# Performance work log

Hardware: AMD Instinct MI355X
Metric: run time of the kernel (lower is better)

Reference implementation:

```python
import jax, jax.numpy as jnp
import numpy as np
import math

H = 16          # attn_heads
DK = 64         # features_dec // attn_heads
NEG = -1e9      # additive causal mask value
EPS = 1e-6      # LayerNorm eps (annotated transformer)


def get_slopes(n):
    def p2(m):
        start = 2.0 ** (-(2.0 ** (-(math.log2(m) - 3))))
        return [start * start ** i for i in range(m)]
    if math.log2(n).is_integer():
        return p2(n)
    cp = 2 ** math.floor(math.log2(n))
    return p2(cp) + get_slopes(2 * cp)[0::2][: n - cp]


def setup_inputs() -> dict:
    key = jax.random.key(0)
    ks = jax.random.split(key, 12)
    B, S, FT, FDZ, FDEC, FD = 8, 1024, 16, 768, 1024, 16

    def lin(k, out_d, in_d):
        return jax.random.normal(k, (out_d, in_d), jnp.float32) / np.float32(np.sqrt(in_d))

    return {
        "z_sample": jax.random.normal(ks[0], (B, FDZ), jnp.float32),
        "r_traj": jax.random.normal(ks[1], (B, S, FT), jnp.float32),
        "dense_w": lin(ks[2], FDEC, FDZ + FT), "dense_b": jnp.zeros((FDEC,), jnp.float32),
        "ln_g": jnp.ones((FDEC,), jnp.float32), "ln_b": jnp.zeros((FDEC,), jnp.float32),
        "wq": lin(ks[3], FDEC, FDEC), "bq": jnp.zeros((FDEC,), jnp.float32),
        "wk": lin(ks[4], FDEC, FDEC), "bk": jnp.zeros((FDEC,), jnp.float32),
        "wv": lin(ks[5], FDEC, FDEC), "bv": jnp.zeros((FDEC,), jnp.float32),
        "wo": lin(ks[6], FDEC, FDEC), "bo": jnp.zeros((FDEC,), jnp.float32),
        "dec_w": lin(ks[7], FD, FDEC), "dec_b": jnp.zeros((FD,), jnp.float32),
    }


def reference(z_sample, r_traj, dense_w, dense_b, ln_g, ln_b,
              wq, bq, wk, bk, wv, bv, wo, bo, dec_w, dec_b):
    B, S, _ = r_traj.shape
    # concat trajectory features with broadcast latent sample -> [B,S,in_size]
    x = jnp.concatenate(
        [r_traj, jnp.broadcast_to(z_sample[:, None, :], (B, S, z_sample.shape[-1]))], axis=-1)
    x = x @ dense_w.T + dense_b  # [B,S,FDEC]

    # causal additive mask + ALiBi bias: bias[h,i,j] = causal(i,j) + slope_h * j
    slopes = jnp.asarray(get_slopes(H), jnp.float32)
    causal = jnp.triu(jnp.full((S, S), NEG, jnp.float32), k=1)
    bias = causal[None, :, :] + slopes[:, None, None] * jnp.arange(S, dtype=jnp.float32)[None, None, :]  # [H,S,S]

    # pre-norm sublayer: x + attn(LN(x))  (dropout=0 / eval)
    mu = x.mean(-1, keepdims=True)
    var = x.var(-1, keepdims=True)
    xn = ln_g * (x - mu) / jnp.sqrt(var + EPS) + ln_b

    def heads(w, b):
        return (xn @ w.T + b).reshape(B, S, H, DK).transpose(0, 2, 1, 3)  # [B,H,S,DK]

    q, k, v = heads(wq, bq), heads(wk, bk), heads(wv, bv)
    scores = jnp.einsum('bhid,bhjd->bhij', q, k) / np.float32(np.sqrt(DK)) + bias[None]
    attn = jax.nn.softmax(scores, axis=-1)
    o = jnp.einsum('bhij,bhjd->bhid', attn, v).transpose(0, 2, 1, 3).reshape(B, S, H * DK)
    x = x + o @ wo.T + bo

    # decode_state then transpose(-2,-1) -> [B, features_d, S]
    return (x @ dec_w.T + dec_b).transpose(0, 2, 1)
```

## Files before the change

### kernel.cpp

```cpp
#include <hip/hip_runtime.h>

static constexpr int Bn   = 8;
static constexpr int S    = 1024;
static constexpr int FT   = 16;
static constexpr int FDZ  = 768;
static constexpr int INK  = 784;
static constexpr int FDEC = 1024;
static constexpr int M    = Bn * S;
static constexpr int H    = 16;
static constexpr int FD   = 16;

typedef __bf16 bf16x8 __attribute__((ext_vector_type(8)));
typedef float  f32x4  __attribute__((ext_vector_type(4)));

__device__ __forceinline__ unsigned short f2b(float f) {
  return __builtin_bit_cast(unsigned short, static_cast<__bf16>(f));
}
__device__ __forceinline__ float b2f(unsigned short u) {
  return (float)__builtin_bit_cast(__bf16, u);
}

__device__ __forceinline__ void gload16(const void* g, void* l) {
  __builtin_amdgcn_global_load_lds(
      (const __attribute__((address_space(1))) unsigned int*)g,
      (__attribute__((address_space(3))) unsigned int*)l, 16, 0, 0);
}

__global__ __launch_bounds__(256) void k_pre(const float* __restrict__ dnw,
                                             const float* __restrict__ wq,
                                             const float* __restrict__ wk,
                                             const float* __restrict__ wv,
                                             const float* __restrict__ wo,
                                             const float* __restrict__ dcw,
                                             const float* __restrict__ bq,
                                             const float* __restrict__ bk,
                                             const float* __restrict__ bv,
                                             const float* __restrict__ bo,
                                             const float* __restrict__ dcb,
                                             const float* __restrict__ z,
                                             unsigned short* __restrict__ w3,
                                             unsigned short* __restrict__ dwb,
                                             float* __restrict__ b3,
                                             unsigned short* __restrict__ wt16,
                                             float* __restrict__ part,
                                             float* __restrict__ bias2,
                                             float* __restrict__ za) {
  const int bid = blockIdx.x, tid = threadIdx.x;
  const int c = tid * 4;
  if (bid < 3072) {
    const int r = bid;
    const float* src = (r < 1024) ? wq : (r < 2048 ? wk : wv);
    const int rr = r & 1023;
    float4 v = *reinterpret_cast<const float4*>(&src[(size_t)rr * 1024 + c]);
    unsigned short o4[4] = {f2b(v.x), f2b(v.y), f2b(v.z), f2b(v.w)};
    *reinterpret_cast<uint2*>(&w3[(size_t)r * 1024 + c]) = *reinterpret_cast<uint2*>(o4);
  } else if (bid < 3088) {
    const int r = bid - 3072;
    float4 v = *reinterpret_cast<const float4*>(&dcw[(size_t)r * 1024 + c]);
    unsigned short o4[4] = {f2b(v.x), f2b(v.y), f2b(v.z), f2b(v.w)};
    *reinterpret_cast<uint2*>(&dwb[(size_t)r * 1024 + c]) = *reinterpret_cast<uint2*>(o4);
  } else if (bid < 3091) {
    const int r = bid - 3088;
    const float* s = (r == 0) ? bq : (r == 1 ? bk : bv);
    *reinterpret_cast<float4*>(&b3[r * 1024 + c]) =
        *reinterpret_cast<const float4*>(&s[c]);
  } else if (bid < 3155) {
    const int idx = (bid - 3091) * 256 + tid;
    const int k = idx >> 10, cc = idx & 1023;
    wt16[k * 1024 + cc] = f2b(dnw[(size_t)cc * INK + k]);
  } else if (bid < 3219) {
    const int kb = bid - 3155;
    const int k0 = kb * 16;
    float4 wv4[16];
#pragma unroll
    for (int k = 0; k < 16; k++)
      wv4[k] = *reinterpret_cast<const float4*>(&wo[(size_t)(k0 + k) * 1024 + c]);
#pragma unroll
    for (int i = 0; i < 16; i++) {
      float4 a = make_float4(0.f, 0.f, 0.f, 0.f);
#pragma unroll
      for (int k = 0; k < 16; k++) {
        float d = dcw[i * 1024 + k0 + k];
        a.x += d * wv4[k].x; a.y += d * wv4[k].y;
        a.z += d * wv4[k].z; a.w += d * wv4[k].w;
      }
      *reinterpret_cast<float4*>(&part[((size_t)kb * 16 + i) * 1024 + c]) = a;
    }
  } else if (bid < 3220) {
    const int lane = tid & 63, w = tid >> 6;
    for (int q = 0; q < 4; q++) {
      int f = w * 4 + q;
      const float* dp = &dcw[(size_t)f * 1024];
      float s = 0.f;
#pragma unroll
      for (int t = 0; t < 16; t++) {
        int k = lane + t * 64;
        s += dp[k] * bo[k];
      }
      for (int off = 32; off; off >>= 1) s += __shfl_down(s, off);
      if (lane == 0) bias2[f] = s + dcb[f];
    }
  } else {
    const int lane = tid & 63, w = tid >> 6;
    const int idx = (bid - 3220) * 4 + w;
    const int col = idx >> 3, b = idx & 7;
    const float* wp = &dnw[(size_t)col * INK + FT];
    const float* zp = &z[b * FDZ];
    float s = 0.f;
#pragma unroll
    for (int i = 0; i < 12; i++) {
      int k = lane + i * 64;
      s += wp[k] * zp[k];
    }
    for (int off = 32; off; off >>= 1) s += __shfl_down(s, off);
    if (lane == 0) za[b * 1024 + col] = s;
  }
}

__global__ __launch_bounds__(256) void k_dln(const float* __restrict__ rt,
                                             const float* __restrict__ za,
                                             const float* __restrict__ dnb,
                                             const float* __restrict__ lng,
                                             const float* __restrict__ lnb,
                                             const unsigned short* __restrict__ wt16g,
                                             const float* __restrict__ part,
                                             unsigned short* __restrict__ xres,
                                             unsigned short* __restrict__ xn,
                                             unsigned short* __restrict__ wcombb) {
  const int tid = threadIdx.x;
  if (blockIdx.x >= 2048) {
    const int idx = (blockIdx.x - 2048) * 256 + tid;
    float s = 0.f;
#pragma unroll 8
    for (int kb = 0; kb < 64; kb++) s += part[(size_t)kb * 16384 + idx];
    wcombb[idx] = f2b(s);
    return;
  }
  __shared__ unsigned short wt[16 * 1024];
  __shared__ float ss[4], qq[4];
  const int lane = tid & 63, wv = tid >> 6;
  const int c0 = tid * 4;
#pragma unroll
  for (int i = 0; i < 8; i++)
    reinterpret_cast<uint4*>(wt)[tid + 256 * i] =
        reinterpret_cast<const uint4*>(wt16g)[tid + 256 * i];
  const float4 bv  = *reinterpret_cast<const float4*>(&dnb[c0]);
  const float4 gv  = *reinterpret_cast<const float4*>(&lng[c0]);
  const float4 bev = *reinterpret_cast<const float4*>(&lnb[c0]);
  __syncthreads();

  for (int r = 0; r < 4; ++r) {
    const int m = blockIdx.x * 4 + r;
    const int b = m >> 10;
    float rtv[16];
    {
      float4 t0 = *reinterpret_cast<const float4*>(&rt[m * 16 + 0]);
      float4 t1 = *reinterpret_cast<const float4*>(&rt[m * 16 + 4]);
      float4 t2 = *reinterpret_cast<const float4*>(&rt[m * 16 + 8]);
      float4 t3 = *reinterpret_cast<const float4*>(&rt[m * 16 + 12]);
      rtv[0]=t0.x; rtv[1]=t0.y; rtv[2]=t0.z; rtv[3]=t0.w;
      rtv[4]=t1.x; rtv[5]=t1.y; rtv[6]=t1.z; rtv[7]=t1.w;
      rtv[8]=t2.x; rtv[9]=t2.y; rtv[10]=t2.z; rtv[11]=t2.w;
      rtv[12]=t3.x; rtv[13]=t3.y; rtv[14]=t3.z; rtv[15]=t3.w;
    }
    float4 zav = *reinterpret_cast<const float4*>(&za[b * 1024 + c0]);
    float acc[4] = {zav.x + bv.x, zav.y + bv.y, zav.z + bv.z, zav.w + bv.w};
#pragma unroll
    for (int k = 0; k < 16; ++k) {
      uint2 wraw = *reinterpret_cast<const uint2*>(&wt[k * 1024 + c0]);
      const unsigned short* wp = reinterpret_cast<const unsigned short*>(&wraw);
      float rk = rtv[k];
      acc[0] += rk * b2f(wp[0]);
      acc[1] += rk * b2f(wp[1]);
      acc[2] += rk * b2f(wp[2]);
      acc[3] += rk * b2f(wp[3]);
    }
    float s = acc[0] + acc[1] + acc[2] + acc[3];
    float q = acc[0]*acc[0] + acc[1]*acc[1] + acc[2]*acc[2] + acc[3]*acc[3];
    for (int off = 32; off; off >>= 1) { s += __shfl_down(s, off); q += __shfl_down(q, off); }
    if (lane == 0) { ss[wv] = s; qq[wv] = q; }
    __syncthreads();
    float St = ss[0] + ss[1] + ss[2] + ss[3];
    float Qt = qq[0] + qq[1] + qq[2] + qq[3];
    float mu  = St * (1.f / 1024.f);
    float var = Qt * (1.f / 1024.f) - mu * mu;
    float rstd = rsqrtf(var + 1e-6f);
    unsigned short xo[4], no[4];
    xo[0] = f2b(acc[0]); no[0] = f2b(gv.x * (acc[0] - mu) * rstd + bev.x);
    xo[1] = f2b(acc[1]); no[1] = f2b(gv.y * (acc[1] - mu) * rstd + bev.y);
    xo[2] = f2b(acc[2]); no[2] = f2b(gv.z * (acc[2] - mu) * rstd + bev.z);
    xo[3] = f2b(acc[3]); no[3] = f2b(gv.w * (acc[3] - mu) * rstd + bev.w);
    *reinterpret_cast<uint2*>(&xres[(size_t)m * 1024 + c0]) = *reinterpret_cast<uint2*>(xo);
    *reinterpret_cast<uint2*>(&xn[(size_t)m * 1024 + c0])   = *reinterpret_cast<uint2*>(no);
    __syncthreads();
  }
}

template<int EPI>
__global__ __launch_bounds__(256, 3) void k_gemm1(const unsigned short* __restrict__ A, int lda,
                                                  const unsigned short* __restrict__ Bw, int ldb,
                                                  int K, int N,
                                                  const float* __restrict__ bias,
                                                  unsigned short* __restrict__ Cb) {
  __shared__ __align__(16) unsigned short As[3 * 128 * 32];
  __shared__ __align__(16) unsigned short Bs[3 * 128 * 32];
  const int tid = threadIdx.x, lane = tid & 63, w = tid >> 6;
  const int wr = w >> 1, wc = w & 1;
  const int lr = lane & 15, lg = lane >> 4;

  const int xcd = blockIdx.x & 7;
  const int j   = blockIdx.x >> 3;
  const int m0  = (xcd * 8 + (j & 7)) * 128;
  const int n0  = (j >> 3) * 128;

  const int nt = K >> 5;

  const int g0 = tid;
  const int r0g = g0 >> 2, c0g = (g0 & 3) ^ ((r0g >> 1) & 3);
  const int g1 = tid + 256;
  const int r1g = g1 >> 2, c1g = (g1 & 3) ^ ((r1g >> 1) & 3);
  const unsigned short* srcA0 = A + (size_t)(m0 + r0g) * lda + c0g * 8;
  const unsigned short* srcA1 = A + (size_t)(m0 + r1g) * lda + c1g * 8;
  const unsigned short* srcB0 = Bw + (size_t)(n0 + r0g) * ldb + c0g * 8;
  const unsigned short* srcB1 = Bw + (size_t)(n0 + r1g) * ldb + c1g * 8;
  const int d0 = (w * 64) * 8;
  const int d1 = (256 + w * 64) * 8;

  int offA[4], offB[4];
#pragma unroll
  for (int mi = 0; mi < 4; mi++) {
    int r = wr * 64 + mi * 16 + lr;
    offA[mi] = r * 32 + (lg ^ ((r >> 1) & 3)) * 8;
  }
#pragma unroll
  for (int ni = 0; ni < 4; ni++) {
    int r = wc * 64 + ni * 16 + lr;
    offB[ni] = r * 32 + (lg ^ ((r >> 1) & 3)) * 8;
  }

  f32x4 acc[4][4];
#pragma unroll
  for (int i = 0; i < 4; i++)
#pragma unroll
    for (int j2 = 0; j2 < 4; j2++)
#pragma unroll
      for (int e = 0; e < 4; e++) acc[i][j2][e] = 0.f;

  auto stage = [&](int tt) {
    const int sl = tt % 3;
    const size_t ko = (size_t)tt * 32;
    gload16(srcA0 + ko, &As[sl * 4096 + d0]);
    gload16(srcA1 + ko, &As[sl * 4096 + d1]);
    gload16(srcB0 + ko, &Bs[sl * 4096 + d0]);
    gload16(srcB1 + ko, &Bs[sl * 4096 + d1]);
  };
  auto compute = [&](int tt) {
    const int sl = (tt % 3) * 4096;
    bf16x8 af[4], bfr[4];
#pragma unroll
    for (int mi = 0; mi < 4; mi++)
      af[mi] = *reinterpret_cast<const bf16x8*>(&As[sl + offA[mi]]);
#pragma unroll
    for (int ni = 0; ni < 4; ni++)
      bfr[ni] = *reinterpret_cast<const bf16x8*>(&Bs[sl + offB[ni]]);
    __builtin_amdgcn_s_setprio(1);
#pragma unroll
    for (int mi = 0; mi < 4; mi++)
#pragma unroll
      for (int ni = 0; ni < 4; ni++)
        acc[mi][ni] = __builtin_amdgcn_mfma_f32_16x16x32_bf16(af[mi], bfr[ni], acc[mi][ni], 0, 0, 0);
    __builtin_amdgcn_s_setprio(0);
  };

  stage(0); stage(1);

  int t = 0;
  for (; t < nt - 2; ++t) {
    asm volatile("s_waitcnt vmcnt(4)" ::: "memory");
    __builtin_amdgcn_s_barrier();
    stage(t + 2);
    compute(t);
  }
  asm volatile("s_waitcnt vmcnt(4)" ::: "memory");
  __builtin_amdgcn_s_barrier();
  compute(t); ++t;
  asm volatile("s_waitcnt vmcnt(0)" ::: "memory");
  __builtin_amdgcn_s_barrier();
  compute(t);

#pragma unroll
  for (int mi = 0; mi < 4; mi++)
#pragma unroll
    for (int ni = 0; ni < 4; ni++) {
      int col = n0 + wc * 64 + ni * 16 + lr;
      float bv = bias ? bias[col] : 0.f;
#pragma unroll
      for (int jj = 0; jj < 4; jj++) {
        int row = m0 + wr * 64 + mi * 16 + lg * 4 + jj;
        float v = acc[mi][ni][jj] + bv;
        Cb[(size_t)row * N + col] = f2b(v);
      }
    }
}

__global__ __launch_bounds__(512, 4) void k_attn(const unsigned short* __restrict__ qkv,
                                                 unsigned short* __restrict__ o) {
  __shared__ unsigned short Ks[2][64][72];
  __shared__ unsigned short Vt[2][64][72];
  __shared__ unsigned short Pl[8][16][72];
  const int tid = threadIdx.x, lane = tid & 63, w = tid >> 6;
  const int bh = blockIdx.x, b = bh >> 4, h = bh & 15;
  const int lr = lane & 15, lg = lane >> 4, lg4 = lg * 4;
  const int krow = tid >> 3, c8 = (tid & 7) << 3;
  const int kb8 = krow >> 3, kl = krow & 7, vq = tid & 7;
  const float slope2 = exp2f(-0.5f * (float)(h + 1)) * 1.44269504f;
  const float sc2 = 0.125f * 1.44269504f;

  const int y = blockIdx.y;
  const int qloA = y * 128 + w * 16;
  const int qloB = (7 - y) * 128 + w * 16;
  const int qaA = qloA + lr, qaB = qloB + lr;

  bf16x8 qfA0, qfA1, qfB0, qfB1;
  {
    const unsigned short* qp = &qkv[(size_t)(b * 1024 + qloA + lr) * 3072 + h * 64];
    qfA0 = *reinterpret_cast<const bf16x8*>(qp + lg * 8);
    qfA1 = *reinterpret_cast<const bf16x8*>(qp + 32 + lg * 8);
    const unsigned short* qp2 = &qkv[(size_t)(b * 1024 + qloB + lr) * 3072 + h * 64];
    qfB0 = *reinterpret_cast<const bf16x8*>(qp2 + lg * 8);
    qfB1 = *reinterpret_cast<const bf16x8*>(qp2 + 32 + lg * 8);
  }
  float mrunA = -3.0e38f, lrunA = 0.f, mrunB = -3.0e38f, lrunB = 0.f;
  f32x4 accOA[4], accOB[4];
  for (int dn = 0; dn < 4; dn++)
    for (int e = 0; e < 4; e++) { accOA[dn][e] = 0.f; accOB[dn][e] = 0.f; }

  const int nt = 16 - 2 * y;

  auto proc = [&](int kb, int cb, int qlo, int qa, float& mrun, float& lrun,
                  f32x4 (&accO)[4], bf16x8 qf0, bf16x8 qf1) {
    f32x4 sf[4];
    for (int kn = 0; kn < 4; kn++) {
      f32x4 zz;
      for (int e = 0; e < 4; e++) zz[e] = 0.f;
      bf16x8 kf0 = *reinterpret_cast<const bf16x8*>(&Ks[cb][kn * 16 + lr][lg * 8]);
      bf16x8 kf1 = *reinterpret_cast<const bf16x8*>(&Ks[cb][kn * 16 + lr][32 + lg * 8]);
      zz = __builtin_amdgcn_mfma_f32_16x16x32_bf16(kf0, qf0, zz, 0, 0, 0);
      zz = __builtin_amdgcn_mfma_f32_16x16x32_bf16(kf1, qf1, zz, 0, 0, 0);
      sf[kn] = zz;
    }
    const bool needmask = (kb + 63 > qlo);
    float sc[4][4];
    float ml = -3.0e38f;
    for (int kn = 0; kn < 4; kn++) {
      float alib = slope2 * (float)(kb + kn * 16 + lg4);
      for (int jj = 0; jj < 4; jj++) {
        float v = fmaf(sf[kn][jj], sc2, alib + slope2 * (float)jj);
        if (needmask && (kb + kn * 16 + lg4 + jj > qa)) v = -3.0e38f;
        sc[kn][jj] = v;
        ml = fmaxf(ml, v);
      }
    }
    ml = fmaxf(ml, __shfl_xor(ml, 16));
    ml = fmaxf(ml, __shfl_xor(ml, 32));
    float mnew = fmaxf(mrun, ml);
    float f = exp2f(mrun - mnew);
    float rs = 0.f;
    for (int kn = 0; kn < 4; kn++) {
      __bf16 pb[4];
      for (int jj = 0; jj < 4; jj++) {
        float pv = exp2f(sc[kn][jj] - mnew);
        rs += pv;
        pb[jj] = (__bf16)pv;
      }
      *reinterpret_cast<uint2*>(&Pl[w][lr][kn * 16 + lg4]) =
          *reinterpret_cast<uint2*>(pb);
    }
    rs += __shfl_xor(rs, 16);
    rs += __shfl_xor(rs, 32);
    lrun = lrun * f + rs;
    mrun = mnew;
    float fj[4];
    for (int jj = 0; jj < 4; jj++) fj[jj] = __shfl(f, (lane & 48) | (lg4 + jj));
    for (int dn = 0; dn < 4; dn++)
      for (int jj = 0; jj < 4; jj++) accO[dn][jj] *= fj[jj];
    asm volatile("s_waitcnt lgkmcnt(0)" ::: "memory");
    for (int ks = 0; ks < 2; ks++) {
      bf16x8 pa = *reinterpret_cast<const bf16x8*>(&Pl[w][lr][ks * 32 + lg * 8]);
      for (int dn = 0; dn < 4; dn++) {
        int d = dn * 16 + lr;
        bf16x8 vb = *reinterpret_cast<const bf16x8*>(
            &Vt[cb][d][(((ks * 4 + lg) ^ (d >> 3)) << 3)]);
        accO[dn] = __builtin_amdgcn_mfma_f32_16x16x32_bf16(pa, vb, accO[dn], 0, 0, 0);
      }
    }
  };

  uint4 kr, vr;
  {
    const size_t base = (size_t)(b * 1024 + krow) * 3072 + h * 64;
    kr = *reinterpret_cast<const uint4*>(&qkv[base + 1024 + c8]);
    vr = *reinterpret_cast<const uint4*>(&qkv[base + 2048 + c8]);
  }
  *reinterpret_cast<uint4*>(&Ks[0][krow][c8]) = kr;
  {
    const unsigned short* vs = reinterpret_cast<const unsigned short*>(&vr);
    for (int jj = 0; jj < 8; jj++)
      Vt[0][c8 + jj][((kb8 ^ vq) << 3) | kl] = vs[jj];
  }
  __syncthreads();

  for (int kt = 0; kt < nt; ++kt) {
    const int kb = kt << 6;
    const int cb = kt & 1, nb = cb ^ 1;
    const bool hn = (kt + 1 < nt);
    if (hn) {
      const size_t base = (size_t)(b * 1024 + kb + 64 + krow) * 3072 + h * 64;
      kr = *reinterpret_cast<const uint4*>(&qkv[base + 1024 + c8]);
      vr = *reinterpret_cast<const uint4*>(&qkv[base + 2048 + c8]);
    }
    if (kb <= qloA + 15)
      proc(kb, cb, qloA, qaA, mrunA, lrunA, accOA, qfA0, qfA1);
    if (hn) {
      *reinterpret_cast<uint4*>(&Ks[nb][krow][c8]) = kr;
      const unsigned short* vs = reinterpret_cast<const unsigned short*>(&vr);
      for (int jj = 0; jj < 8; jj++)
        Vt[nb][c8 + jj][((kb8 ^ vq) << 3) | kl] = vs[jj];
    }
    if (kb <= qloB + 15)
      proc(kb, cb, qloB, qaB, mrunB, lrunB, accOB, qfB0, qfB1);
    __syncthreads();
  }

  float linvA[4], linvB[4];
  for (int jj = 0; jj < 4; jj++) {
    linvA[jj] = 1.f / __shfl(lrunA, (lane & 48) | (lg4 + jj));
    linvB[jj] = 1.f / __shfl(lrunB, (lane & 48) | (lg4 + jj));
  }
  for (int dn = 0; dn < 4; dn++)
    for (int jj = 0; jj < 4; jj++) {
      int d = dn * 16 + lr;
      int rowA = qloA + lg4 + jj;
      o[(size_t)(b * 1024 + rowA) * 1024 + h * 64 + d] = f2b(accOA[dn][jj] * linvA[jj]);
      int rowB = qloB + lg4 + jj;
      o[(size_t)(b * 1024 + rowB) * 1024 + h * 64 + d] = f2b(accOB[dn][jj] * linvB[jj]);
    }
}

__global__ __launch_bounds__(256) void k_dec2(const unsigned short* __restrict__ xres,
                                              const unsigned short* __restrict__ ob,
                                              const unsigned short* __restrict__ dwb,
                                              const unsigned short* __restrict__ wcombb,
                                              const float* __restrict__ bias2,
                                              float* __restrict__ out) {
  const int tid = threadIdx.x, lane = tid & 63, w = tid >> 6;
  const int lr = lane & 15, lg = lane >> 4;
  const int sb = blockIdx.x * 4 + w;
  const int r0 = sb * 16;
  f32x4 acc;
  for (int e = 0; e < 4; e++) acc[e] = 0.f;
  const unsigned short* arow1 = &xres[(size_t)(r0 + lr) * 1024];
  const unsigned short* arow2 = &ob[(size_t)(r0 + lr) * 1024];
  const unsigned short* brow1 = &dwb[(size_t)lr * 1024];
  const unsigned short* brow2 = &wcombb[(size_t)lr * 1024];
  for (int k0 = 0; k0 < 1024; k0 += 32) {
    bf16x8 a1 = *reinterpret_cast<const bf16x8*>(arow1 + k0 + lg * 8);
    bf16x8 b1 = *reinterpret_cast<const bf16x8*>(brow1 + k0 + lg * 8);
    acc = __builtin_amdgcn_mfma_f32_16x16x32_bf16(a1, b1, acc, 0, 0, 0);
    bf16x8 a2 = *reinterpret_cast<const bf16x8*>(arow2 + k0 + lg * 8);
    bf16x8 b2 = *reinterpret_cast<const bf16x8*>(brow2 + k0 + lg * 8);
    acc = __builtin_amdgcn_mfma_f32_16x16x32_bf16(a2, b2, acc, 0, 0, 0);
  }
  const int b = r0 >> 10;
  const int sl = (r0 & 1023) + lg * 4;
  float bias = bias2[lr];
  float4 res;
  res.x = acc[0] + bias; res.y = acc[1] + bias; res.z = acc[2] + bias; res.w = acc[3] + bias;
  *reinterpret_cast<float4*>(&out[(size_t)(b * 16 + lr) * 1024 + sl]) = res;
}

extern "C" void kernel_launch(void* const* d_in, const int* in_sizes, int n_in,
                              void* d_out, int out_size, void* d_ws, size_t ws_size,
                              hipStream_t stream) {
  (void)in_sizes; (void)n_in; (void)out_size;
  const float* z   = (const float*)d_in[0];
  const float* rt  = (const float*)d_in[1];
  const float* dnw = (const float*)d_in[2];
  const float* dnb = (const float*)d_in[3];
  const float* lng = (const float*)d_in[4];
  const float* lnb = (const float*)d_in[5];
  const float* wq  = (const float*)d_in[6];
  const float* bq  = (const float*)d_in[7];
  const float* wk  = (const float*)d_in[8];
  const float* bk  = (const float*)d_in[9];
  const float* wv  = (const float*)d_in[10];
  const float* bv  = (const float*)d_in[11];
  const float* wo  = (const float*)d_in[12];
  const float* bo  = (const float*)d_in[13];
  const float* dcw = (const float*)d_in[14];
  const float* dcb = (const float*)d_in[15];
  float* out = (float*)d_out;

  char* p = (char*)d_ws;
  unsigned short* xres  = (unsigned short*)p; p += (size_t)M * FDEC * 2;
  unsigned short* xn    = (unsigned short*)p; p += (size_t)M * FDEC * 2;
  unsigned short* w3    = (unsigned short*)p; p += (size_t)3 * FDEC * FDEC * 2;
  float* b3             = (float*)p;          p += (size_t)3 * FDEC * 4;
  unsigned short* qkv   = (unsigned short*)p; p += (size_t)M * 3 * FDEC * 2;
  unsigned short* ob    = (unsigned short*)p; p += (size_t)M * FDEC * 2;
  unsigned short* dwb   = (unsigned short*)p; p += (size_t)FD * FDEC * 2;
  unsigned short* wcombb= (unsigned short*)p; p += (size_t)FD * FDEC * 2;
  float* bias2          = (float*)p;          p += (size_t)FD * 4;
  float* za             = (float*)p;          p += (size_t)8 * 1024 * 4;
  unsigned short* wt16  = (unsigned short*)p; p += (size_t)16 * 1024 * 2;
  float* part           = (float*)p;          p += (size_t)64 * FD * FDEC * 4;
  if ((size_t)(p - (char*)d_ws) > ws_size) return;

  k_pre<<<5268, 256, 0, stream>>>(dnw, wq, wk, wv, wo, dcw, bq, bk, bv, bo, dcb, z,
                                  w3, dwb, b3, wt16, part, bias2, za);
  k_dln<<<2112, 256, 0, stream>>>(rt, za, dnb, lng, lnb, wt16, part, xres, xn, wcombb);
  k_gemm1<1><<<(M / 128) * (3 * FDEC / 128), 256, 0, stream>>>(xn, FDEC, w3, FDEC, FDEC, 3 * FDEC, b3, qkv);
  k_attn<<<dim3(Bn * H, 4), 512, 0, stream>>>(qkv, ob);
  k_dec2<<<M / 64, 256, 0, stream>>>(xres, ob, dwb, wcombb, bias2, out);
}
```

Before: 159.9 us.

## Fuse folded output projection into attention epilogue with atomic accumulation

The attention kernel now applies the folded Wo·dec weight (kept in fp32) directly to its per-head output tile and atomically adds the 16-feature result into the final output. The bf16 attention output buffer in global memory and its reread by the decode kernel go away. A separate decode kernel for the residual path runs earlier and writes the base output, which the attention kernel then adds into. The cost is shuffle reductions and 16 passes per tile in the epilogue, plus atomic contention across heads and nondeterministic summation order.

```diff
diff --git a/kernel.cpp b/kernel.cpp
--- a/kernel.cpp
+++ b/kernel.cpp
@@ -126,14 +126,14 @@
                                              const float* __restrict__ part,
                                              unsigned short* __restrict__ xres,
                                              unsigned short* __restrict__ xn,
-                                             unsigned short* __restrict__ wcombb) {
+                                             float* __restrict__ wcombf) {
   const int tid = threadIdx.x;
   if (blockIdx.x >= 2048) {
     const int idx = (blockIdx.x - 2048) * 256 + tid;
     float s = 0.f;
 #pragma unroll 8
     for (int kb = 0; kb < 64; kb++) s += part[(size_t)kb * 16384 + idx];
-    wcombb[idx] = f2b(s);
+    wcombf[idx] = s;
     return;
   }
   __shared__ unsigned short wt[16 * 1024];
@@ -304,10 +304,12 @@
 }
 
 __global__ __launch_bounds__(512, 4) void k_attn(const unsigned short* __restrict__ qkv,
-                                                 unsigned short* __restrict__ o) {
+                                                 const float* __restrict__ wcf,
+                                                 float* __restrict__ out) {
   __shared__ unsigned short Ks[2][64][72];
   __shared__ unsigned short Vt[2][64][72];
   __shared__ unsigned short Pl[8][16][72];
+  __shared__ float wcs[16 * 64];
   const int tid = threadIdx.x, lane = tid & 63, w = tid >> 6;
   const int bh = blockIdx.x, b = bh >> 4, h = bh & 15;
   const int lr = lane & 15, lg = lane >> 4, lg4 = lg * 4;
@@ -315,6 +317,9 @@
   const int kb8 = krow >> 3, kl = krow & 7, vq = tid & 7;
   const float slope2 = exp2f(-0.5f * (float)(h + 1)) * 1.44269504f;
   const float sc2 = 0.125f * 1.44269504f;
+
+  wcs[tid]       = wcf[(tid >> 6) * 1024 + h * 64 + (tid & 63)];
+  wcs[tid + 512] = wcf[((tid >> 6) + 8) * 1024 + h * 64 + (tid & 63)];
 
   const int y = blockIdx.y;
   const int qloA = y * 128 + w * 16;
@@ -432,25 +437,38 @@
     __syncthreads();
   }
 
-  float linvA[4], linvB[4];
-  for (int jj = 0; jj < 4; jj++) {
-    linvA[jj] = 1.f / __shfl(lrunA, (lane & 48) | (lg4 + jj));
-    linvB[jj] = 1.f / __shfl(lrunB, (lane & 48) | (lg4 + jj));
-  }
-  for (int dn = 0; dn < 4; dn++)
+  auto epi = [&](int qlo, float lrun, f32x4 (&accO)[4]) {
+    float linv[4];
+    for (int jj = 0; jj < 4; jj++)
+      linv[jj] = 1.f / __shfl(lrun, (lane & 48) | (lg4 + jj));
+    float pw[4];
+    for (int f = 0; f < 16; ++f) {
+      float p[4] = {0.f, 0.f, 0.f, 0.f};
+#pragma unroll
+      for (int dn = 0; dn < 4; dn++) {
+        float wv = wcs[f * 64 + dn * 16 + lr];
+#pragma unroll
+        for (int jj = 0; jj < 4; jj++) p[jj] += accO[dn][jj] * wv;
+      }
+      for (int off = 1; off < 16; off <<= 1)
+#pragma unroll
+        for (int jj = 0; jj < 4; jj++) p[jj] += __shfl_xor(p[jj], off);
+      if (lr == f)
+#pragma unroll
+        for (int jj = 0; jj < 4; jj++) pw[jj] = p[jj] * linv[jj];
+    }
+#pragma unroll
     for (int jj = 0; jj < 4; jj++) {
-      int d = dn * 16 + lr;
-      int rowA = qloA + lg4 + jj;
-      o[(size_t)(b * 1024 + rowA) * 1024 + h * 64 + d] = f2b(accOA[dn][jj] * linvA[jj]);
-      int rowB = qloB + lg4 + jj;
-      o[(size_t)(b * 1024 + rowB) * 1024 + h * 64 + d] = f2b(accOB[dn][jj] * linvB[jj]);
-    }
-}
-
-__global__ __launch_bounds__(256) void k_dec2(const unsigned short* __restrict__ xres,
-                                              const unsigned short* __restrict__ ob,
+      int row = qlo + lg4 + jj;
+      atomicAdd(&out[(size_t)b * 16384 + lr * 1024 + row], pw[jj]);
+    }
+  };
+  epi(qloA, lrunA, accOA);
+  epi(qloB, lrunB, accOB);
+}
+
+__global__ __launch_bounds__(256) void k_decx(const unsigned short* __restrict__ xres,
                                               const unsigned short* __restrict__ dwb,
-                                              const unsigned short* __restrict__ wcombb,
                                               const float* __restrict__ bias2,
                                               float* __restrict__ out) {
   const int tid = threadIdx.x, lane = tid & 63, w = tid >> 6;
@@ -459,17 +477,12 @@
   const int r0 = sb * 16;
   f32x4 acc;
   for (int e = 0; e < 4; e++) acc[e] = 0.f;
-  const unsigned short* arow1 = &xres[(size_t)(r0 + lr) * 1024];
-  const unsigned short* arow2 = &ob[(size_t)(r0 + lr) * 1024];
-  const unsigned short* brow1 = &dwb[(size_t)lr * 1024];
-  const unsigned short* brow2 = &wcombb[(size_t)lr * 1024];
+  const unsigned short* arow = &xres[(size_t)(r0 + lr) * 1024];
+  const unsigned short* brow = &dwb[(size_t)lr * 1024];
   for (int k0 = 0; k0 < 1024; k0 += 32) {
-    bf16x8 a1 = *reinterpret_cast<const bf16x8*>(arow1 + k0 + lg * 8);
-    bf16x8 b1 = *reinterpret_cast<const bf16x8*>(brow1 + k0 + lg * 8);
-    acc = __builtin_amdgcn_mfma_f32_16x16x32_bf16(a1, b1, acc, 0, 0, 0);
-    bf16x8 a2 = *reinterpret_cast<const bf16x8*>(arow2 + k0 + lg * 8);
-    bf16x8 b2 = *reinterpret_cast<const bf16x8*>(brow2 + k0 + lg * 8);
-    acc = __builtin_amdgcn_mfma_f32_16x16x32_bf16(a2, b2, acc, 0, 0, 0);
+    bf16x8 af = *reinterpret_cast<const bf16x8*>(arow + k0 + lg * 8);
+    bf16x8 bf = *reinterpret_cast<const bf16x8*>(brow + k0 + lg * 8);
+    acc = __builtin_amdgcn_mfma_f32_16x16x32_bf16(af, bf, acc, 0, 0, 0);
   }
   const int b = r0 >> 10;
   const int sl = (r0 & 1023) + lg * 4;
@@ -507,9 +520,8 @@
   unsigned short* w3    = (unsigned short*)p; p += (size_t)3 * FDEC * FDEC * 2;
   float* b3             = (float*)p;          p += (size_t)3 * FDEC * 4;
   unsigned short* qkv   = (unsigned short*)p; p += (size_t)M * 3 * FDEC * 2;
-  unsigned short* ob    = (unsigned short*)p; p += (size_t)M * FDEC * 2;
   unsigned short* dwb   = (unsigned short*)p; p += (size_t)FD * FDEC * 2;
-  unsigned short* wcombb= (unsigned short*)p; p += (size_t)FD * FDEC * 2;
+  float* wcombf         = (float*)p;          p += (size_t)FD * FDEC * 4;
   float* bias2          = (float*)p;          p += (size_t)FD * 4;
   float* za             = (float*)p;          p += (size_t)8 * 1024 * 4;
   unsigned short* wt16  = (unsigned short*)p; p += (size_t)16 * 1024 * 2;
@@ -518,8 +530,8 @@
 
   k_pre<<<5268, 256, 0, stream>>>(dnw, wq, wk, wv, wo, dcw, bq, bk, bv, bo, dcb, z,
                                   w3, dwb, b3, wt16, part, bias2, za);
-  k_dln<<<2112, 256, 0, stream>>>(rt, za, dnb, lng, lnb, wt16, part, xres, xn, wcombb);
+  k_dln<<<2112, 256, 0, stream>>>(rt, za, dnb, lng, lnb, wt16, part, xres, xn, wcombf);
+  k_decx<<<M / 64, 256, 0, stream>>>(xres, dwb, bias2, out);
   k_gemm1<1><<<(M / 128) * (3 * FDEC / 128), 256, 0, stream>>>(xn, FDEC, w3, FDEC, FDEC, 3 * FDEC, b3, qkv);
-  k_attn<<<dim3(Bn * H, 4), 512, 0, stream>>>(qkv, ob);
-  k_dec2<<<M / 64, 256, 0, stream>>>(xres, ob, dwb, wcombb, bias2, out);
-}
+  k_attn<<<dim3(Bn * H, 4), 512, 0, stream>>>(qkv, wcombf, out);
+}
```

Result: slower. 180.0 us (+12.6%).
